# Optimization experiments

Hardware: AMD Instinct MI355X
Metric: run time of the kernel (lower is better)

Reference implementation:

```python
import jax, jax.numpy as jnp
import numpy as np

D_MODEL = 1024
NUM_HEADS = 16
SEQ_LEN = 2048
BATCH = 2
THETA = 10000.0


def apply_rope(x, positions, theta):
    # x: [..., seq, d_k]; positions: [seq]
    dk = x.shape[-1]
    half = dk // 2
    k = jnp.arange(half, dtype=jnp.float32)
    inv_freq = theta ** (-2.0 * k / dk)                 # [half]
    ang = positions.astype(jnp.float32)[:, None] * inv_freq  # [seq, half]
    cos, sin = jnp.cos(ang), jnp.sin(ang)
    xe = x[..., 0::2]   # even members of adjacent pairs
    xo = x[..., 1::2]
    out_e = cos * xe - sin * xo
    out_o = sin * xe + cos * xo
    # interleave pairs back: [..., seq, half, 2] -> [..., seq, dk]
    return jnp.stack([out_e, out_o], axis=-1).reshape(x.shape)


def setup_inputs() -> dict:
    key = jax.random.key(0)
    kx, kq, kk, kv, ko = jax.random.split(key, 5)
    sig = 1.0 / np.sqrt(D_MODEL)
    def tn(k):
        return jnp.clip(jax.random.normal(k, (D_MODEL, D_MODEL), jnp.float32), -3.0, 3.0) * sig
    return {
        "x": jax.random.normal(kx, (BATCH, SEQ_LEN, D_MODEL), jnp.float32),
        "q_proj_weight": tn(kq),
        "k_proj_weight": tn(kk),
        "v_proj_weight": tn(kv),
        "o_proj_weight": tn(ko),
        "token_positions": jnp.arange(SEQ_LEN, dtype=jnp.int32),
    }


def reference(x, q_proj_weight, k_proj_weight, v_proj_weight, o_proj_weight, token_positions):
    h = NUM_HEADS
    d = x.shape[-1]
    dh = d // h
    seq = x.shape[-2]
    Wq = q_proj_weight.reshape(h, dh, d)
    Wk = k_proj_weight.reshape(h, dh, d)
    Wv = v_proj_weight.reshape(h, dh, d)
    Q = jnp.einsum('bsd,hed->bhse', x, Wq)
    K = jnp.einsum('bsd,hed->bhse', x, Wk)
    V = jnp.einsum('bsd,hed->bhse', x, Wv)
    Q = apply_rope(Q, token_positions, THETA)
    K = apply_rope(K, token_positions, THETA)
    scores = jnp.einsum('bhqe,bhke->bhqk', Q, K) / jnp.sqrt(jnp.float32(dh))
    mask = jnp.tril(jnp.ones((seq, seq), dtype=bool))
    scores = jnp.where(mask, scores, -jnp.inf)
    probs = jax.nn.softmax(scores, axis=-1)
    att = jnp.einsum('bhqk,bhke->bhqe', probs, V)       # [b, h, s, dh]
    att = att.transpose(0, 2, 1, 3).reshape(x.shape[0], seq, d)  # concat heads
    return jnp.einsum('bsh,dh->bsd', att, o_proj_weight)
```

## Files before the change

### kernel.cpp

```cpp
#include <hip/hip_runtime.h>
#include <hip/hip_bf16.h>
#include <cstdint>
#include <cstddef>

#define DEV static __device__ __forceinline__

typedef __bf16 bf16x8 __attribute__((ext_vector_type(8)));
typedef float f32x4 __attribute__((ext_vector_type(4)));
typedef unsigned short u16;

static constexpr int BATCH = 2, SEQ = 2048, DM = 1024, NH = 16, DH = 64;
static constexpr int Kdim = 1024;
static constexpr int BS = BATCH * SEQ;

DEV u16 f2b(float f) {
  uint32_t u = __builtin_bit_cast(uint32_t, f);
  u += 0x7FFFu + ((u >> 16) & 1u);
  return (u16)(u >> 16);
}

DEV void gload_lds16(const void* g, void* l) {
  __builtin_amdgcn_global_load_lds((const __attribute__((address_space(1))) void*)g,
                                   (__attribute__((address_space(3))) void*)l, 16, 0, 0);
}

DEV void plswap32(uint32_t& a, uint32_t& b) {
  asm("v_permlane32_swap_b32 %0, %1" : "+v"(a), "+v"(b));
}
DEV void plswap16(uint32_t& a, uint32_t& b) {
  asm("v_permlane16_swap_b32 %0, %1" : "+v"(a), "+v"(b));
}

__global__ __launch_bounds__(256) void cast_all(const float* __restrict__ x,
    const float* __restrict__ wq, const float* __restrict__ wk,
    const float* __restrict__ wv, const float* __restrict__ wo,
    const int* __restrict__ pos,
    u16* __restrict__ xb, u16* __restrict__ wqb, u16* __restrict__ wkb,
    u16* __restrict__ wvb, u16* __restrict__ wob, float2* __restrict__ tab) {
  const int NX = (BATCH * SEQ * DM) / 4;
  const int NW = (DM * DM) / 4;
  const int NT = SEQ * 32;
  int i = blockIdx.x * blockDim.x + threadIdx.x;
  const int stride = gridDim.x * blockDim.x;
  for (; i < NX + 4 * NW + NT; i += stride) {
    if (i < NX + 4 * NW) {
      const float* src; u16* dst; int off;
      if (i < NX) { src = x; dst = xb; off = i; }
      else {
        const int j = i - NX, seg = j >> 18;
        off = j & (NW - 1);
        src = seg == 0 ? wq : seg == 1 ? wk : seg == 2 ? wv : wo;
        dst = seg == 0 ? wqb : seg == 1 ? wkb : seg == 2 ? wvb : wob;
      }
      float4 v = ((const float4*)src)[off];
      ushort4 o;
      o.x = f2b(v.x); o.y = f2b(v.y); o.z = f2b(v.z); o.w = f2b(v.w);
      ((ushort4*)dst)[off] = o;
    } else {
      const int t = i - NX - 4 * NW;
      const int s = t >> 5, j = t & 31;
      const float ang = (float)pos[s] * exp2f((float)j * -0.4152410118609203f);
      float sn, cs;
      sincosf(ang, &sn, &cs);
      tab[t] = make_float2(cs, sn);
    }
  }
}

template <bool OUTF32>
DEV void gemm_core64(const u16* __restrict__ A, const u16* __restrict__ Bm,
                     void* __restrict__ Cout, int ldC, int m0, int n0,
                     u16* __restrict__ As, u16* __restrict__ Bs) {
  const int tid = threadIdx.x;
  const int lane = tid & 63, wid = tid >> 6;
  const int wr = (wid >> 1) * 64, wc = (wid & 1) * 32;
  const int frow = lane & 15, fgrp = lane >> 4;
  constexpr int NK = Kdim / 32;
  f32x4 acc[4][2] = {};

  const int c0 = tid, c1 = tid + 256;
  const int ra0 = c0 >> 2, sa0 = (c0 & 3) ^ ((ra0 >> 1) & 3);
  const int ra1 = c1 >> 2, sa1 = (c1 & 3) ^ ((ra1 >> 1) & 3);
  const size_t gA0 = (size_t)(m0 + ra0) * Kdim + sa0 * 8;
  const size_t gA1 = (size_t)(m0 + ra1) * Kdim + sa1 * 8;
  const size_t gB0 = (size_t)(n0 + ra0) * Kdim + sa0 * 8;

#define GSTAGE(bufi, kofs)                                                      \
  do {                                                                          \
    gload_lds16(A + gA0 + (kofs), As + (bufi) * 4096 + wid * 512);              \
    gload_lds16(A + gA1 + (kofs), As + (bufi) * 4096 + wid * 512 + 2048);       \
    gload_lds16(Bm + gB0 + (kofs), Bs + (bufi) * 2048 + wid * 512);             \
  } while (0)

  GSTAGE(0, 0);
  for (int kt = 0; kt < NK; ++kt) {
    const int buf = kt & 1;
    if (kt + 1 < NK) {
      GSTAGE((kt + 1) & 1, (kt + 1) * 32);
      asm volatile("s_waitcnt vmcnt(3)" ::: "memory");
    } else {
      asm volatile("s_waitcnt vmcnt(0)" ::: "memory");
    }
    __builtin_amdgcn_s_barrier();

    bf16x8 af[4], bfr[2];
#pragma unroll
    for (int i = 0; i < 4; ++i) {
      const int ra = wr + i * 16 + frow;
      af[i] = *(const bf16x8*)((const char*)(As + buf * 4096) + ra * 64 +
                               ((fgrp ^ ((ra >> 1) & 3)) * 16));
    }
#pragma unroll
    for (int f = 0; f < 2; ++f) {
      const int rb = wc + f * 16 + frow;
      bfr[f] = *(const bf16x8*)((const char*)(Bs + buf * 2048) + rb * 64 +
                                ((fgrp ^ ((rb >> 1) & 3)) * 16));
    }
#pragma unroll
    for (int mi = 0; mi < 4; ++mi)
#pragma unroll
      for (int f = 0; f < 2; ++f)
        acc[mi][f] = __builtin_amdgcn_mfma_f32_16x16x32_bf16(af[mi], bfr[f], acc[mi][f], 0, 0, 0);

    __builtin_amdgcn_s_barrier();
  }
#undef GSTAGE

  const int colb = n0 + wc + frow;
  const int rowb = m0 + wr + fgrp * 4;
#pragma unroll
  for (int mi = 0; mi < 4; ++mi)
#pragma unroll
    for (int f = 0; f < 2; ++f)
#pragma unroll
      for (int r = 0; r < 4; ++r) {
        const int row = rowb + mi * 16 + r;
        const int col = colb + f * 16;
        const float v = acc[mi][f][r];
        if (OUTF32) ((float*)Cout)[(size_t)row * ldC + col] = v;
        else        ((u16*)Cout)[(size_t)row * ldC + col] = f2b(v);
      }
}

__global__ __launch_bounds__(256) void gemm_qk_fused(const u16* __restrict__ xb,
    const u16* __restrict__ wq, const u16* __restrict__ wk,
    u16* __restrict__ Qb, u16* __restrict__ Kb, const float2* __restrict__ tab) {
  __shared__ u16 As[2][4096], Bq[2][2048], Bk[2][2048];
  const int f = blockIdx.x;
  const int xcd = f & 7, j = f >> 3;
  const int m0 = (xcd * 4 + (j >> 4)) * 128, n0 = (j & 15) * 64;

  const int tid = threadIdx.x;
  const int lane = tid & 63, wid = tid >> 6;
  const int wr = (wid >> 1) * 64, wc = (wid & 1) * 32;
  const int frow = lane & 15, fgrp = lane >> 4;
  constexpr int NK = Kdim / 32;
  f32x4 accQ[4][2] = {}, accK[4][2] = {};

  const int c0 = tid, c1 = tid + 256;
  const int ra0 = c0 >> 2, sa0 = (c0 & 3) ^ ((ra0 >> 1) & 3);
  const int ra1 = c1 >> 2, sa1 = (c1 & 3) ^ ((ra1 >> 1) & 3);
  const size_t gA0 = (size_t)(m0 + ra0) * Kdim + sa0 * 8;
  const size_t gA1 = (size_t)(m0 + ra1) * Kdim + sa1 * 8;
  const size_t gB0 = (size_t)(n0 + ra0) * Kdim + sa0 * 8;

#define QKSTAGE(bufi, kofs)                                                     \
  do {                                                                          \
    gload_lds16(xb + gA0 + (kofs), &As[bufi][0] + wid * 512);                   \
    gload_lds16(xb + gA1 + (kofs), &As[bufi][0] + wid * 512 + 2048);            \
    gload_lds16(wq + gB0 + (kofs), &Bq[bufi][0] + wid * 512);                   \
    gload_lds16(wk + gB0 + (kofs), &Bk[bufi][0] + wid * 512);                   \
  } while (0)

  QKSTAGE(0, 0);
  for (int kt = 0; kt < NK; ++kt) {
    const int buf = kt & 1;
    if (kt + 1 < NK) {
      QKSTAGE((kt + 1) & 1, (kt + 1) * 32);
      asm volatile("s_waitcnt vmcnt(4)" ::: "memory");
    } else {
      asm volatile("s_waitcnt vmcnt(0)" ::: "memory");
    }
    __builtin_amdgcn_s_barrier();

    bf16x8 af[4], bq[2], bk[2];
#pragma unroll
    for (int i = 0; i < 4; ++i) {
      const int ra = wr + i * 16 + frow;
      af[i] = *(const bf16x8*)((const char*)&As[buf][0] + ra * 64 +
                               ((fgrp ^ ((ra >> 1) & 3)) * 16));
    }
#pragma unroll
    for (int f2 = 0; f2 < 2; ++f2) {
      const int rb = wc + f2 * 16 + frow;
      const int off = rb * 64 + ((fgrp ^ ((rb >> 1) & 3)) * 16);
      bq[f2] = *(const bf16x8*)((const char*)&Bq[buf][0] + off);
      bk[f2] = *(const bf16x8*)((const char*)&Bk[buf][0] + off);
    }
#pragma unroll
    for (int mi = 0; mi < 4; ++mi)
#pragma unroll
      for (int f2 = 0; f2 < 2; ++f2) {
        accQ[mi][f2] = __builtin_amdgcn_mfma_f32_16x16x32_bf16(af[mi], bq[f2], accQ[mi][f2], 0, 0, 0);
        accK[mi][f2] = __builtin_amdgcn_mfma_f32_16x16x32_bf16(af[mi], bk[f2], accK[mi][f2], 0, 0, 0);
      }

    __builtin_amdgcn_s_barrier();
  }
#undef QKSTAGE

  const int colb = n0 + wc + frow;
  const int rowb = m0 + wr + fgrp * 4;
#pragma unroll
  for (int mi = 0; mi < 4; ++mi)
#pragma unroll
    for (int f2 = 0; f2 < 2; ++f2) {
      const int col = colb + f2 * 16;
      const int jj = (col & 63) >> 1;
      const int odd = col & 1;
#pragma unroll
      for (int r = 0; r < 4; ++r) {
        const int row = rowb + mi * 16 + r;
        const float2 cs_ = tab[(row & (SEQ - 1)) * 32 + jj];
        const float qv = accQ[mi][f2][r];
        const float qp = __shfl_xor(qv, 1);
        const float kv = accK[mi][f2][r];
        const float kp = __shfl_xor(kv, 1);
        float oq = odd ? fmaf(cs_.y, qp, cs_.x * qv) : fmaf(cs_.x, qv, -cs_.y * qp);
        float ok = odd ? fmaf(cs_.y, kp, cs_.x * kv) : fmaf(cs_.x, kv, -cs_.y * kp);
        oq *= 0.18033688011112043f;
        Qb[(size_t)row * DM + col] = f2b(oq);
        Kb[(size_t)row * DM + col] = f2b(ok);
      }
    }
}

__global__ __launch_bounds__(256) void gemm_vt(const u16* __restrict__ wv,
                                               const u16* __restrict__ xb,
                                               u16* __restrict__ Vtb) {
  __shared__ u16 As[2][4096], Bs[2][2048];
  const int f = blockIdx.x;
  const int xcd = f & 7, j = f >> 3;
  const int m0 = xcd * 128, n0 = j * 64;
  gemm_core64<false>(wv, xb, Vtb, BS, m0, n0, &As[0][0], &Bs[0][0]);
}

__global__ __launch_bounds__(256) void gemm_o(const u16* __restrict__ attb,
                                              const u16* __restrict__ wob,
                                              float* __restrict__ out) {
  __shared__ u16 As[2][4096], Bs[2][2048];
  const int f = blockIdx.x;
  const int xcd = f & 7, k = f >> 3;
  const int grp = xcd * 8 + (k >> 3);
  const int m0 = (grp >> 1) * 128;
  const int n0 = ((grp & 1) * 8 + (k & 7)) * 64;
  gemm_core64<true>(attb, wob, out, DM, m0, n0, &As[0][0], &Bs[0][0]);
}

__global__ __launch_bounds__(512, 4) void attn_kernel(const u16* __restrict__ Qb,
                                                      const u16* __restrict__ Kb,
                                                      const u16* __restrict__ Vtb,
                                                      u16* __restrict__ attb) {
  __shared__ __align__(16) unsigned char SM[73728];
  float* Of = (float*)SM;
  float* Ld = (float*)(SM + 65536);

  const int tid = threadIdx.x, lane = tid & 63, wid = tid >> 6;
  const int qh = wid >> 2, kq = wid & 3;
  const int flat = (int)blockIdx.x + 16 * (int)blockIdx.y;
  const int orig = (flat & 7) * 64 + (flat >> 3);
  const int xq = orig & 15;
  const int bh = orig >> 4;
  const int b = bh >> 4, h = bh & 15;
  const size_t base_bh = ((size_t)b * SEQ) * DM + h * DH;
  const int frow = lane & 15, fgrp = lane >> 4;
  const int kq32 = kq * 32;
  const int swz = (frow & 7) << 4;

  const u16* Ksrcs[2];
  const u16* Vsrcs[2];
#pragma unroll
  for (int i = 0; i < 2; ++i) {
    const int c = tid + i * 512;
    const int rk = c >> 3, s8 = (c & 7) ^ (rk & 7);
    Ksrcs[i] = Kb + base_bh + (size_t)rk * DM + s8 * 8;
    const int rv = c >> 4, s16 = (c & 15) ^ (rv & 7);
    Vsrcs[i] = Vtb + (size_t)(h * DH + rv) * BS + (size_t)b * SEQ + s16 * 8;
  }
  const int rq = tid >> 3, sq = (tid & 7) ^ (rq & 7);

#pragma unroll 1
  for (int phase = 0; phase < 2; ++phase) {
    const int qt = phase ? xq : 31 - xq;
    const int q0 = qt * 64;
    const int nkv = (qt >> 1) + 1;

    gload_lds16(Qb + base_bh + (size_t)(q0 + rq) * DM + sq * 8, (char*)SM + 65536 + tid * 16);
#pragma unroll
    for (int i = 0; i < 2; ++i) {
      gload_lds16(Ksrcs[i], (char*)SM + i * 8192 + tid * 16);
      gload_lds16(Vsrcs[i], (char*)SM + 32768 + i * 8192 + tid * 16);
    }
    __syncthreads();

    bf16x8 qf[2][2];
#pragma unroll
    for (int qs = 0; qs < 2; ++qs)
#pragma unroll
      for (int ks = 0; ks < 2; ++ks) {
        const int byte = ((qh * 32 + qs * 16 + frow) * 128 + ks * 64 + fgrp * 16) ^ swz;
        qf[qs][ks] = *(const bf16x8*)((const char*)SM + 65536 + byte);
      }

    f32x4 accO[2][4] = {};
    float l_lane[2] = {0.f, 0.f};

    for (int kt = 0; kt < nkv; ++kt) {
      const char* Kc = (const char*)SM + (kt & 1) * 16384;
      const char* Vc = (const char*)SM + 32768 + (kt & 1) * 16384;
      if (kt + 1 < nkv) {
        const size_t kvn = (size_t)(kt + 1) * 128;
        const int nb = (kt + 1) & 1;
#pragma unroll
        for (int i = 0; i < 2; ++i) {
          gload_lds16(Ksrcs[i] + kvn * DM, (char*)SM + nb * 16384 + i * 8192 + tid * 16);
          gload_lds16(Vsrcs[i] + kvn, (char*)SM + 32768 + nb * 16384 + i * 8192 + tid * 16);
        }
      }

      f32x4 sc[2][2] = {};
      __builtin_amdgcn_s_setprio(1);
#pragma unroll
      for (int tc = 0; tc < 2; ++tc)
#pragma unroll
        for (int ks = 0; ks < 2; ++ks) {
          const int byte = ((kq32 + tc * 16 + frow) * 128 + ks * 64 + fgrp * 16) ^ swz;
          const bf16x8 kf = *(const bf16x8*)(Kc + byte);
#pragma unroll
          for (int qs = 0; qs < 2; ++qs)
            sc[qs][tc] = __builtin_amdgcn_mfma_f32_16x16x32_bf16(kf, qf[qs][ks], sc[qs][tc], 0, 0, 0);
        }
      __builtin_amdgcn_s_setprio(0);

      if (kt == nkv - 1) {
        const int kv0 = kt * 128;
#pragma unroll
        for (int qs = 0; qs < 2; ++qs)
#pragma unroll
          for (int tc = 0; tc < 2; ++tc)
#pragma unroll
            for (int r = 0; r < 4; ++r)
              if (kv0 + kq32 + tc * 16 + fgrp * 4 + r > q0 + qh * 32 + qs * 16 + frow)
                sc[qs][tc][r] = -1e30f;
      }

      bf16x8 pf[2];
#pragma unroll
      for (int qs = 0; qs < 2; ++qs) {
        const float p00 = exp2f(sc[qs][0][0]), p01 = exp2f(sc[qs][0][1]);
        const float p02 = exp2f(sc[qs][0][2]), p03 = exp2f(sc[qs][0][3]);
        const float p10 = exp2f(sc[qs][1][0]), p11 = exp2f(sc[qs][1][1]);
        const float p12 = exp2f(sc[qs][1][2]), p13 = exp2f(sc[qs][1][3]);
        l_lane[qs] += ((p00 + p01) + (p02 + p03)) + ((p10 + p11) + (p12 + p13));
        union { __bf16 bb[2]; uint32_t uu; } c00, c01, c10, c11;
        c00.bb[0] = (__bf16)p00; c00.bb[1] = (__bf16)p01;
        c01.bb[0] = (__bf16)p02; c01.bb[1] = (__bf16)p03;
        c10.bb[0] = (__bf16)p10; c10.bb[1] = (__bf16)p11;
        c11.bb[0] = (__bf16)p12; c11.bb[1] = (__bf16)p13;
        uint32_t a0 = c00.uu, a1 = c01.uu, b0 = c10.uu, b1 = c11.uu;
        plswap32(a0, b0); plswap16(a0, b0);
        plswap32(a1, b1); plswap16(a1, b1);
        union { uint32_t w[4]; bf16x8 v; } pk;
        pk.w[0] = a0; pk.w[1] = a1; pk.w[2] = b0; pk.w[3] = b1;
        pf[qs] = pk.v;
      }

      __builtin_amdgcn_s_setprio(1);
#pragma unroll
      for (int te = 0; te < 4; ++te) {
        const int byte = ((te * 16 + frow) * 256 + kq * 64 + fgrp * 16) ^ swz;
        const bf16x8 vf = *(const bf16x8*)(Vc + byte);
#pragma unroll
        for (int qs = 0; qs < 2; ++qs)
          accO[qs][te] = __builtin_amdgcn_mfma_f32_16x16x32_bf16(pf[qs], vf, accO[qs][te], 0, 0, 0);
      }
      __builtin_amdgcn_s_setprio(0);
      __syncthreads();
    }

    float* myOf = Of + wid * 2048;
#pragma unroll
    for (int qs = 0; qs < 2; ++qs)
#pragma unroll
      for (int te = 0; te < 4; ++te)
#pragma unroll
        for (int r = 0; r < 4; ++r)
          myOf[(qs * 16 + fgrp * 4 + r) * 64 + te * 16 + frow] = accO[qs][te][r];
#pragma unroll
    for (int qs = 0; qs < 2; ++qs) {
      l_lane[qs] += __shfl_xor(l_lane[qs], 16);
      l_lane[qs] += __shfl_xor(l_lane[qs], 32);
    }
    if (fgrp == 0) {
#pragma unroll
      for (int qs = 0; qs < 2; ++qs) Ld[wid * 32 + qs * 16 + frow] = l_lane[qs];
    }
    __syncthreads();

#pragma unroll
    for (int ii = 0; ii < 2; ++ii) {
      const int ql = wid * 8 + fgrp * 2 + ii;
      const int hh = ql >> 5, qlh = ql & 31;
      f32x4 s = {};
      float lq = 0.f;
#pragma unroll
      for (int j = 0; j < 4; ++j) {
        s += *(const f32x4*)(Of + (hh * 4 + j) * 2048 + qlh * 64 + frow * 4);
        lq += Ld[(hh * 4 + j) * 32 + qlh];
      }
      const float inv = 1.0f / lq;
      ushort4 o;
      o.x = f2b(s[0] * inv); o.y = f2b(s[1] * inv);
      o.z = f2b(s[2] * inv); o.w = f2b(s[3] * inv);
      *(ushort4*)(attb + base_bh + (size_t)(q0 + ql) * DM + frow * 4) = o;
    }
    __syncthreads();
  }
}

extern "C" void kernel_launch(void* const* d_in, const int* in_sizes, int n_in,
                              void* d_out, int out_size, void* d_ws, size_t ws_size,
                              hipStream_t stream) {
  const float* x  = (const float*)d_in[0];
  const float* wq = (const float*)d_in[1];
  const float* wk = (const float*)d_in[2];
  const float* wv = (const float*)d_in[3];
  const float* wo = (const float*)d_in[4];
  const int* pos  = (const int*)d_in[5];
  float* out = (float*)d_out;
  (void)in_sizes; (void)n_in; (void)out_size; (void)ws_size;

  char* ws = (char*)d_ws;
  const size_t MB = 1024 * 1024;
  u16* xb   = (u16*)(ws);
  u16* wqb  = (u16*)(ws + 8 * MB);
  u16* wkb  = (u16*)(ws + 10 * MB);
  u16* wvb  = (u16*)(ws + 12 * MB);
  u16* wob  = (u16*)(ws + 14 * MB);
  u16* Qb   = (u16*)(ws + 16 * MB);
  u16* Kb   = (u16*)(ws + 24 * MB);
  u16* Vtb  = (u16*)(ws + 32 * MB);
  u16* attb = (u16*)(ws + 40 * MB);
  float2* tab = (float2*)(ws + 40 * MB);

  cast_all<<<2048, 256, 0, stream>>>(x, wq, wk, wv, wo, pos, xb, wqb, wkb, wvb, wob, tab);
  gemm_qk_fused<<<512, 256, 0, stream>>>(xb, wqb, wkb, Qb, Kb, tab);
  gemm_vt<<<512, 256, 0, stream>>>(wvb, xb, Vtb);
  attn_kernel<<<dim3(16, 32), 512, 0, stream>>>(Qb, Kb, Vtb, attb);
  gemm_o<<<512, 256, 0, stream>>>(attb, wob, out);
}
```

Before: 118.4 us.

## Use 4 waves per attention block, each covering all 64 queries

The attention kernel drops from 8 waves (2 query halves × 4 KV slices) to 4 waves, each handling all 64 query rows over its own 32-key slice of the 128-key tile. Every K/V fragment read from LDS now feeds twice as many MFMAs, and cross-wave reduction partners are fewer. The cost is double the accumulator and score registers per wave, half as many waves to hide latency, and launch bounds that fall from 512×4 to 256×2, which may reduce occupancy.

New measurement: 117.3 us. About the same (-0.8%).

```diff
diff --git a/kernel.cpp b/kernel.cpp
--- a/kernel.cpp
+++ b/kernel.cpp
@@ -257,16 +257,16 @@
   gemm_core64<true>(attb, wob, out, DM, m0, n0, &As[0][0], &Bs[0][0]);
 }
 
-__global__ __launch_bounds__(512, 4) void attn_kernel(const u16* __restrict__ Qb,
+__global__ __launch_bounds__(256, 2) void attn_kernel(const u16* __restrict__ Qb,
                                                       const u16* __restrict__ Kb,
                                                       const u16* __restrict__ Vtb,
                                                       u16* __restrict__ attb) {
   __shared__ __align__(16) unsigned char SM[73728];
+  u16* Qs = (u16*)(SM + 65536);
   float* Of = (float*)SM;
   float* Ld = (float*)(SM + 65536);
 
   const int tid = threadIdx.x, lane = tid & 63, wid = tid >> 6;
-  const int qh = wid >> 2, kq = wid & 3;
   const int flat = (int)blockIdx.x + 16 * (int)blockIdx.y;
   const int orig = (flat & 7) * 64 + (flat >> 3);
   const int xq = orig & 15;
@@ -274,20 +274,22 @@
   const int b = bh >> 4, h = bh & 15;
   const size_t base_bh = ((size_t)b * SEQ) * DM + h * DH;
   const int frow = lane & 15, fgrp = lane >> 4;
-  const int kq32 = kq * 32;
+  const int w32 = wid * 32;
   const int swz = (frow & 7) << 4;
 
-  const u16* Ksrcs[2];
-  const u16* Vsrcs[2];
-#pragma unroll
-  for (int i = 0; i < 2; ++i) {
-    const int c = tid + i * 512;
+  const u16* Ksrcs[4];
+  const u16* Vsrcs[4];
+#pragma unroll
+  for (int i = 0; i < 4; ++i) {
+    const int c = tid + i * 256;
     const int rk = c >> 3, s8 = (c & 7) ^ (rk & 7);
     Ksrcs[i] = Kb + base_bh + (size_t)rk * DM + s8 * 8;
     const int rv = c >> 4, s16 = (c & 15) ^ (rv & 7);
     Vsrcs[i] = Vtb + (size_t)(h * DH + rv) * BS + (size_t)b * SEQ + s16 * 8;
   }
-  const int rq = tid >> 3, sq = (tid & 7) ^ (rq & 7);
+  const int cq0 = tid, cq1 = tid + 256;
+  const int rq0 = cq0 >> 3, sq0 = (cq0 & 7) ^ (rq0 & 7);
+  const int rq1 = cq1 >> 3, sq1 = (cq1 & 7) ^ (rq1 & 7);
 
 #pragma unroll 1
   for (int phase = 0; phase < 2; ++phase) {
@@ -295,25 +297,26 @@
     const int q0 = qt * 64;
     const int nkv = (qt >> 1) + 1;
 
-    gload_lds16(Qb + base_bh + (size_t)(q0 + rq) * DM + sq * 8, (char*)SM + 65536 + tid * 16);
-#pragma unroll
-    for (int i = 0; i < 2; ++i) {
-      gload_lds16(Ksrcs[i], (char*)SM + i * 8192 + tid * 16);
-      gload_lds16(Vsrcs[i], (char*)SM + 32768 + i * 8192 + tid * 16);
+    gload_lds16(Qb + base_bh + (size_t)(q0 + rq0) * DM + sq0 * 8, (char*)SM + 65536 + tid * 16);
+    gload_lds16(Qb + base_bh + (size_t)(q0 + rq1) * DM + sq1 * 8, (char*)SM + 69632 + tid * 16);
+#pragma unroll
+    for (int i = 0; i < 4; ++i) {
+      gload_lds16(Ksrcs[i], (char*)SM + wid * 1024 + i * 4096);
+      gload_lds16(Vsrcs[i], (char*)SM + 32768 + wid * 1024 + i * 4096);
     }
     __syncthreads();
 
-    bf16x8 qf[2][2];
-#pragma unroll
-    for (int qs = 0; qs < 2; ++qs)
+    bf16x8 qf[4][2];
+#pragma unroll
+    for (int qs = 0; qs < 4; ++qs)
 #pragma unroll
       for (int ks = 0; ks < 2; ++ks) {
-        const int byte = ((qh * 32 + qs * 16 + frow) * 128 + ks * 64 + fgrp * 16) ^ swz;
-        qf[qs][ks] = *(const bf16x8*)((const char*)SM + 65536 + byte);
-      }
-
-    f32x4 accO[2][4] = {};
-    float l_lane[2] = {0.f, 0.f};
+        const int byte = ((qs * 16 + frow) * 128 + ks * 64 + fgrp * 16) ^ swz;
+        qf[qs][ks] = *(const bf16x8*)((const char*)Qs + byte);
+      }
+
+    f32x4 accO[4][4] = {};
+    float l_lane[4] = {0.f, 0.f, 0.f, 0.f};
 
     for (int kt = 0; kt < nkv; ++kt) {
       const char* Kc = (const char*)SM + (kt & 1) * 16384;
@@ -322,22 +325,22 @@
         const size_t kvn = (size_t)(kt + 1) * 128;
         const int nb = (kt + 1) & 1;
 #pragma unroll
-        for (int i = 0; i < 2; ++i) {
-          gload_lds16(Ksrcs[i] + kvn * DM, (char*)SM + nb * 16384 + i * 8192 + tid * 16);
-          gload_lds16(Vsrcs[i] + kvn, (char*)SM + 32768 + nb * 16384 + i * 8192 + tid * 16);
+        for (int i = 0; i < 4; ++i) {
+          gload_lds16(Ksrcs[i] + kvn * DM, (char*)SM + nb * 16384 + wid * 1024 + i * 4096);
+          gload_lds16(Vsrcs[i] + kvn, (char*)SM + 32768 + nb * 16384 + wid * 1024 + i * 4096);
         }
       }
 
-      f32x4 sc[2][2] = {};
+      f32x4 sc[4][2] = {};
       __builtin_amdgcn_s_setprio(1);
 #pragma unroll
       for (int tc = 0; tc < 2; ++tc)
 #pragma unroll
         for (int ks = 0; ks < 2; ++ks) {
-          const int byte = ((kq32 + tc * 16 + frow) * 128 + ks * 64 + fgrp * 16) ^ swz;
+          const int byte = ((w32 + tc * 16 + frow) * 128 + ks * 64 + fgrp * 16) ^ swz;
           const bf16x8 kf = *(const bf16x8*)(Kc + byte);
 #pragma unroll
-          for (int qs = 0; qs < 2; ++qs)
+          for (int qs = 0; qs < 4; ++qs)
             sc[qs][tc] = __builtin_amdgcn_mfma_f32_16x16x32_bf16(kf, qf[qs][ks], sc[qs][tc], 0, 0, 0);
         }
       __builtin_amdgcn_s_setprio(0);
@@ -345,18 +348,18 @@
       if (kt == nkv - 1) {
         const int kv0 = kt * 128;
 #pragma unroll
-        for (int qs = 0; qs < 2; ++qs)
+        for (int qs = 0; qs < 4; ++qs)
 #pragma unroll
           for (int tc = 0; tc < 2; ++tc)
 #pragma unroll
             for (int r = 0; r < 4; ++r)
-              if (kv0 + kq32 + tc * 16 + fgrp * 4 + r > q0 + qh * 32 + qs * 16 + frow)
+              if (kv0 + w32 + tc * 16 + fgrp * 4 + r > q0 + qs * 16 + frow)
                 sc[qs][tc][r] = -1e30f;
       }
 
-      bf16x8 pf[2];
-#pragma unroll
-      for (int qs = 0; qs < 2; ++qs) {
+      bf16x8 pf[4];
+#pragma unroll
+      for (int qs = 0; qs < 4; ++qs) {
         const float p00 = exp2f(sc[qs][0][0]), p01 = exp2f(sc[qs][0][1]);
         const float p02 = exp2f(sc[qs][0][2]), p03 = exp2f(sc[qs][0][3]);
         const float p10 = exp2f(sc[qs][1][0]), p11 = exp2f(sc[qs][1][1]);
@@ -378,51 +381,53 @@
       __builtin_amdgcn_s_setprio(1);
 #pragma unroll
       for (int te = 0; te < 4; ++te) {
-        const int byte = ((te * 16 + frow) * 256 + kq * 64 + fgrp * 16) ^ swz;
+        const int byte = ((te * 16 + frow) * 256 + wid * 64 + fgrp * 16) ^ swz;
         const bf16x8 vf = *(const bf16x8*)(Vc + byte);
 #pragma unroll
-        for (int qs = 0; qs < 2; ++qs)
+        for (int qs = 0; qs < 4; ++qs)
           accO[qs][te] = __builtin_amdgcn_mfma_f32_16x16x32_bf16(pf[qs], vf, accO[qs][te], 0, 0, 0);
       }
       __builtin_amdgcn_s_setprio(0);
       __syncthreads();
     }
 
-    float* myOf = Of + wid * 2048;
-#pragma unroll
-    for (int qs = 0; qs < 2; ++qs)
+    float* myOf = Of + wid * 4096;
+#pragma unroll
+    for (int qs = 0; qs < 4; ++qs)
 #pragma unroll
       for (int te = 0; te < 4; ++te)
 #pragma unroll
         for (int r = 0; r < 4; ++r)
           myOf[(qs * 16 + fgrp * 4 + r) * 64 + te * 16 + frow] = accO[qs][te][r];
 #pragma unroll
-    for (int qs = 0; qs < 2; ++qs) {
+    for (int qs = 0; qs < 4; ++qs) {
       l_lane[qs] += __shfl_xor(l_lane[qs], 16);
       l_lane[qs] += __shfl_xor(l_lane[qs], 32);
     }
     if (fgrp == 0) {
 #pragma unroll
-      for (int qs = 0; qs < 2; ++qs) Ld[wid * 32 + qs * 16 + frow] = l_lane[qs];
+      for (int qs = 0; qs < 4; ++qs) Ld[wid * 64 + qs * 16 + frow] = l_lane[qs];
     }
     __syncthreads();
 
-#pragma unroll
-    for (int ii = 0; ii < 2; ++ii) {
-      const int ql = wid * 8 + fgrp * 2 + ii;
-      const int hh = ql >> 5, qlh = ql & 31;
-      f32x4 s = {};
-      float lq = 0.f;
-#pragma unroll
-      for (int j = 0; j < 4; ++j) {
-        s += *(const f32x4*)(Of + (hh * 4 + j) * 2048 + qlh * 64 + frow * 4);
-        lq += Ld[(hh * 4 + j) * 32 + qlh];
-      }
-      const float inv = 1.0f / lq;
-      ushort4 o;
-      o.x = f2b(s[0] * inv); o.y = f2b(s[1] * inv);
-      o.z = f2b(s[2] * inv); o.w = f2b(s[3] * inv);
-      *(ushort4*)(attb + base_bh + (size_t)(q0 + ql) * DM + frow * 4) = o;
+    {
+      const int qlb = wid * 16 + fgrp * 4;
+#pragma unroll
+      for (int i = 0; i < 4; ++i) {
+        const int ql = qlb + i;
+        f32x4 s = {};
+#pragma unroll
+        for (int wv = 0; wv < 4; ++wv) {
+          const f32x4 t = *(const f32x4*)(Of + wv * 4096 + ql * 64 + frow * 4);
+          s += t;
+        }
+        const float lq = ((Ld[ql] + Ld[64 + ql]) + (Ld[128 + ql] + Ld[192 + ql]));
+        const float inv = 1.0f / lq;
+        ushort4 o;
+        o.x = f2b(s[0] * inv); o.y = f2b(s[1] * inv);
+        o.z = f2b(s[2] * inv); o.w = f2b(s[3] * inv);
+        *(ushort4*)(attb + base_bh + (size_t)(q0 + ql) * DM + frow * 4) = o;
+      }
     }
     __syncthreads();
   }
@@ -456,6 +461,6 @@
   cast_all<<<2048, 256, 0, stream>>>(x, wq, wk, wv, wo, pos, xb, wqb, wkb, wvb, wob, tab);
   gemm_qk_fused<<<512, 256, 0, stream>>>(xb, wqb, wkb, Qb, Kb, tab);
   gemm_vt<<<512, 256, 0, stream>>>(wvb, xb, Vtb);
-  attn_kernel<<<dim3(16, 32), 512, 0, stream>>>(Qb, Kb, Vtb, attb);
+  attn_kernel<<<dim3(16, 32), 256, 0, stream>>>(Qb, Kb, Vtb, attb);
   gemm_o<<<512, 256, 0, stream>>>(attb, wob, out);
 }
```
